# Performance work log

Hardware: AMD Instinct MI355X
Metric: run time of the kernel (lower is better)

The kernel has to match this reference:

```python
import jax, jax.numpy as jnp
import numpy as np

D_MODEL = 1024
NUM_HEADS = 16
HEAD_DIM = D_MODEL // NUM_HEADS


def setup_inputs() -> dict:
    key = jax.random.key(0)
    k1, k2, k3, k4, k5 = jax.random.split(key, 5)
    scale = 1.0 / np.sqrt(D_MODEL)
    x = jax.random.normal(k1, (2, 2048, D_MODEL), dtype=jnp.float32)
    Wqkv = jax.random.uniform(k2, (D_MODEL, 3 * D_MODEL), jnp.float32, -scale, scale)
    bqkv = jax.random.uniform(k3, (3 * D_MODEL,), jnp.float32, -scale, scale)
    Wout = jax.random.uniform(k4, (D_MODEL, D_MODEL), jnp.float32, -scale, scale)
    bout = jax.random.uniform(k5, (D_MODEL,), jnp.float32, -scale, scale)
    return {"x": x, "Wqkv": Wqkv, "bqkv": bqkv, "Wout": Wout, "bout": bout}


def reference(x, Wqkv, bqkv, Wout, bout):
    B, S, _ = x.shape
    qkv = x @ Wqkv + bqkv                                   # [B, S, 3*D]
    # reshape to [B, S, H, 3*head_dim] then to [B, H, S, 3*head_dim]
    qkv = qkv.reshape(B, S, NUM_HEADS, 3 * HEAD_DIM).transpose(0, 2, 1, 3)
    q, k, v = jnp.split(qkv, 3, axis=-1)                    # each [B, H, S, hd]
    scaled = jnp.einsum("bhqd,bhkd->bhqk", q, k) / jnp.sqrt(jnp.float32(HEAD_DIM))
    attn = jax.nn.softmax(scaled, axis=-1)                  # [B, H, S, S]
    values = jnp.einsum("bhqk,bhkd->bhqd", attn, v)         # [B, H, S, hd]
    values = values.transpose(0, 2, 1, 3).reshape(B, S, D_MODEL)
    return values @ Wout + bout
```

## Files before the change

kernel.cpp:

```cpp
#include <hip/hip_runtime.h>


typedef __attribute__((ext_vector_type(8)))  short short8;
typedef __attribute__((ext_vector_type(4)))  short short4v;
typedef __attribute__((ext_vector_type(8)))  float float8;
typedef __attribute__((ext_vector_type(4)))  float f32x4;
typedef __attribute__((ext_vector_type(16))) float f32x16;
typedef __attribute__((ext_vector_type(4)))  int   int4v;

#define D_MODEL 1024
#define NHEAD   16
#define HD      64
#define SEQ     2048
#define N3      (3*D_MODEL)
#define MB      (1024*1024)

static __device__ __forceinline__ float bf2f(short s) {
    unsigned u = ((unsigned)(unsigned short)s) << 16;
    return __builtin_bit_cast(float, u);
}
static __device__ __forceinline__ short f2bf(float f) {
    unsigned u = __builtin_bit_cast(unsigned, f);
    u = (u + 0x7fff + ((u >> 16) & 1)) >> 16;
    return (short)u;
}
static __device__ __forceinline__ unsigned pkbf(float a, float b) {
    unsigned ua = __builtin_bit_cast(unsigned, a);
    ua = (ua + 0x7fff + ((ua >> 16) & 1)) >> 16;
    unsigned ub = __builtin_bit_cast(unsigned, b);
    ub = (ub + 0x7fff + ((ub >> 16) & 1)) & 0xffff0000u;
    return ua | ub;
}
static __device__ __forceinline__ unsigned cvtpk(float a, float b) {
    unsigned r;
    asm("v_cvt_pk_bf16_f32 %0, %1, %2" : "=v"(r) : "v"(a), "v"(b));
    return r;
}
static __device__ __forceinline__ void gl16(const short* g, short* l) {
    __builtin_amdgcn_global_load_lds(
        (const __attribute__((address_space(1))) unsigned int*)g,
        (__attribute__((address_space(3))) unsigned int*)l, 16, 0, 0);
}

__global__ __launch_bounds__(256) void prep(
    const float* __restrict__ x, const float* __restrict__ Wqkv,
    const float* __restrict__ Wout,
    short* __restrict__ Xh, short* __restrict__ Xl,
    short* __restrict__ Wh, short* __restrict__ Wl,
    short* __restrict__ Woh, short* __restrict__ Wol)
{
    __shared__ float tile[32][33];
    const int bid = blockIdx.x;
    const int tid = threadIdx.x;

    if (bid < 2048) {
        const int i = (bid * 256 + tid) * 8;
        const float8 v = *(const float8*)&x[i];
        short8 h, l;
#pragma unroll
        for (int j = 0; j < 8; ++j) {
            h[j] = f2bf(v[j]);
            l[j] = f2bf(v[j] - bf2f(h[j]));
        }
        *(short8*)&Xh[i] = h;
        *(short8*)&Xl[i] = l;
        return;
    }

    const float* in; short *hi, *lo; int K, N, bx, by;
    if (bid < 5120) {
        const int b2 = bid - 2048;
        in = Wqkv; hi = Wh; lo = Wl; K = D_MODEL; N = N3;
        bx = b2 % 96; by = b2 / 96;
    } else {
        const int b3 = bid - 5120;
        in = Wout; hi = Woh; lo = Wol; K = D_MODEL; N = D_MODEL;
        bx = b3 & 31; by = b3 >> 5;
    }
    const int n0 = bx * 32, k0 = by * 32;
    const int tx = tid & 31, ty = tid >> 5;
#pragma unroll
    for (int i = 0; i < 4; ++i)
        tile[ty + 8*i][tx] = in[(k0 + ty + 8*i) * N + (n0 + tx)];
    __syncthreads();
#pragma unroll
    for (int i = 0; i < 4; ++i) {
        const float v  = tile[tx][ty + 8*i];
        const short vh = f2bf(v);
        const short vl = f2bf(v - bf2f(vh));
        const int idx  = (n0 + ty + 8*i) * K + (k0 + tx);
        hi[idx] = vh;
        lo[idx] = vl;
    }
}

#define QBUF_SH 28672
#define OFF_AL  8192
#define OFF_BH  16384
#define OFF_BL  22528

__global__ __launch_bounds__(512, 2) void qkv_gemm8(
    const short* __restrict__ Xh, const short* __restrict__ Xl,
    const short* __restrict__ Bh, const short* __restrict__ Bl,
    const float* __restrict__ bias,
    short* __restrict__ Qo, short* __restrict__ Ko, short* __restrict__ Vt)
{
    __shared__ __attribute__((aligned(16))) short smem[2 * QBUF_SH];

    const int tid  = threadIdx.x;
    const int wave = tid >> 6, lane = tid & 63;
    const int q4 = lane >> 4, l16 = lane & 15;
    const int wr = wave >> 2, wc = wave & 3;

    const int flat = blockIdx.x;
    const int sw = (flat & 7) * 32 + (flat >> 3);
    const int mt = sw & 15, nt = sw >> 4;
    const int m0 = mt * 256, n0 = nt * 192;

    const short* srcp[7];
#pragma unroll
    for (int j = 0; j < 7; ++j) {
        const int id = j * 512 + tid;
        const short* s;
        if (id < 1024)      { s = &Xh[(size_t)(m0 + (id >> 2)) * D_MODEL + (id & 3) * 8]; }
        else if (id < 2048) { const int c = id - 1024; s = &Xl[(size_t)(m0 + (c >> 2)) * D_MODEL + (c & 3) * 8]; }
        else if (id < 2816) { const int c = id - 2048; s = &Bh[(size_t)(n0 + (c >> 2)) * D_MODEL + (c & 3) * 8]; }
        else                { const int c = id - 2816; s = &Bl[(size_t)(n0 + (c >> 2)) * D_MODEL + (c & 3) * 8]; }
        srcp[j] = s;
    }

    auto stage = [&](int b) {
#pragma unroll
        for (int j = 0; j < 7; ++j) {
            gl16(srcp[j], smem + b * QBUF_SH + (j * 512 + tid) * 8);
            srcp[j] += 32;
        }
    };

    f32x4 acc[8][3];
#pragma unroll
    for (int i = 0; i < 8; ++i)
#pragma unroll
        for (int j = 0; j < 3; ++j) acc[i][j] = (f32x4){0.f, 0.f, 0.f, 0.f};

    stage(0);
    asm volatile("s_waitcnt vmcnt(0)" ::: "memory");
    __builtin_amdgcn_s_barrier();

    for (int t = 0; t < 32; ++t) {
        const int cur = t & 1;
        const short* base = smem + cur * QBUF_SH;
        const short* Ah_s = base;
        const short* Al_s = base + OFF_AL;
        const short* Bh_s = base + OFF_BH;
        const short* Bl_s = base + OFF_BL;

        short8 bhf[3], blf[3];
#pragma unroll
        for (int p = 0; p < 4; ++p) {
            const int r0 = (wr * 128 + (2*p)   * 16 + l16) * 32 + q4 * 8;
            const int r1 = (wr * 128 + (2*p+1) * 16 + l16) * 32 + q4 * 8;
            const short8 a0h = *(const short8*)(Ah_s + r0);
            const short8 a0l = *(const short8*)(Al_s + r0);
            const short8 a1h = *(const short8*)(Ah_s + r1);
            const short8 a1l = *(const short8*)(Al_s + r1);
            if (p == 0) {
#pragma unroll
                for (int n = 0; n < 3; ++n) {
                    const int rb = (wc * 48 + n * 16 + l16) * 32 + q4 * 8;
                    bhf[n] = *(const short8*)(Bh_s + rb);
                    blf[n] = *(const short8*)(Bl_s + rb);
                }
                if (t < 31) stage(cur ^ 1);
            }
            __builtin_amdgcn_s_barrier();
            asm volatile("s_waitcnt lgkmcnt(0)" ::: "memory");
            __builtin_amdgcn_sched_barrier(0);
            __builtin_amdgcn_s_setprio(1);
#pragma unroll
            for (int n = 0; n < 3; ++n) {
                acc[2*p][n]   = __builtin_amdgcn_mfma_f32_16x16x32_bf16(a0h, bhf[n], acc[2*p][n],   0, 0, 0);
                acc[2*p][n]   = __builtin_amdgcn_mfma_f32_16x16x32_bf16(a0h, blf[n], acc[2*p][n],   0, 0, 0);
                acc[2*p][n]   = __builtin_amdgcn_mfma_f32_16x16x32_bf16(a0l, bhf[n], acc[2*p][n],   0, 0, 0);
                acc[2*p+1][n] = __builtin_amdgcn_mfma_f32_16x16x32_bf16(a1h, bhf[n], acc[2*p+1][n], 0, 0, 0);
                acc[2*p+1][n] = __builtin_amdgcn_mfma_f32_16x16x32_bf16(a1h, blf[n], acc[2*p+1][n], 0, 0, 0);
                acc[2*p+1][n] = __builtin_amdgcn_mfma_f32_16x16x32_bf16(a1l, bhf[n], acc[2*p+1][n], 0, 0, 0);
            }
            __builtin_amdgcn_s_setprio(0);
            if (p == 3) asm volatile("s_waitcnt vmcnt(0)" ::: "memory");
            __builtin_amdgcn_s_barrier();
        }
    }

    const float SCALE_Q = 0.125f * 1.4426950408889634f;
#pragma unroll
    for (int tj = 0; tj < 3; ++tj) {
        const int jj = wc * 48 + tj * 16 + l16;
        const int n  = nt * 192 + jj;
        const float bv = bias[n];
#pragma unroll
        for (int ti = 0; ti < 8; ++ti) {
            const int mb = m0 + wr * 128 + ti * 16 + q4 * 4;
            const int b = mb >> 11;
            const int s = mb & 2047;
            const int bh_ = b * NHEAD + nt;
            if (jj >= 128) {
                short4v v4;
#pragma unroll
                for (int r = 0; r < 4; ++r) v4[r] = f2bf(acc[ti][tj][r] + bv);
                *(short4v*)&Vt[(bh_ * HD + (jj - 128)) * SEQ + s] = v4;
            } else if (jj < 64) {
#pragma unroll
                for (int r = 0; r < 4; ++r)
                    Qo[(bh_ * SEQ + s + r) * HD + jj] = f2bf((acc[ti][tj][r] + bv) * SCALE_Q);
            } else {
#pragma unroll
                for (int r = 0; r < 4; ++r)
                    Ko[(bh_ * SEQ + s + r) * HD + (jj - 64)] = f2bf(acc[ti][tj][r] + bv);
            }
        }
    }
}

__global__ __launch_bounds__(256, 2) void attn_tscore(
    const short* __restrict__ Q, const short* __restrict__ K,
    const short* __restrict__ Vt,
    short* __restrict__ Ch, short* __restrict__ Cl)
{
    __shared__ __attribute__((aligned(16))) char smem[36864];
    short (*Ks)[72] = (short(*)[72])smem;
    short (*Vs)[72] = (short(*)[72])(smem + 18432);

    const int bh = blockIdx.x;
    const int qb = blockIdx.y;
    const int bi = bh >> 4, hi_ = bh & 15;

    const short* Qp  = Q  + bh * SEQ * HD;
    const short* Kp  = K  + bh * SEQ * HD;
    const short* Vtp = Vt + bh * HD * SEQ;

    const int tid  = threadIdx.x;
    const int wave = tid >> 6, lane = tid & 63;
    const int l5 = lane & 31, hf = lane >> 5;
    const int q0w = qb * 128 + wave * 32;

    short8 qf[4];
#pragma unroll
    for (int c = 0; c < 4; ++c)
        qf[c] = *(const short8*)&Qp[(q0w + l5) * HD + c * 16 + hf * 8];

    f32x16 oacc0 = (f32x16)(0.f), oacc1 = (f32x16)(0.f);
    float m = -1.0e30f, l = 0.f;

    const int sr = tid >> 2;
    const int sc = (tid & 3) * 16;

    short8 kr0 = *(const short8*)&Kp[sr * HD + sc];
    short8 kr1 = *(const short8*)&Kp[sr * HD + sc + 8];
    short8 vr0 = *(const short8*)&Vtp[sr * SEQ + sc];
    short8 vr1 = *(const short8*)&Vtp[sr * SEQ + sc + 8];
    *(short8*)&Ks[sr][sc]     = kr0;
    *(short8*)&Ks[sr][sc + 8] = kr1;
    *(short8*)&Vs[sr][sc]     = vr0;
    *(short8*)&Vs[sr][sc + 8] = vr1;
    __syncthreads();

    for (int kc = 0; kc < 32; ++kc) {
        const int buf = (kc & 1) << 6;

        if (kc < 31) {
            const int nkb = (kc + 1) << 6;
            kr0 = *(const short8*)&Kp[(nkb + sr) * HD + sc];
            kr1 = *(const short8*)&Kp[(nkb + sr) * HD + sc + 8];
            vr0 = *(const short8*)&Vtp[sr * SEQ + nkb + sc];
            vr1 = *(const short8*)&Vtp[sr * SEQ + nkb + sc + 8];
        }

        f32x16 s0 = (f32x16)(0.f), s1 = (f32x16)(0.f);
#pragma unroll
        for (int c = 0; c < 4; ++c) {
            const short8 ka0 = *(const short8*)&Ks[buf + l5][c * 16 + hf * 8];
            const short8 ka1 = *(const short8*)&Ks[buf + 32 + l5][c * 16 + hf * 8];
            s0 = __builtin_amdgcn_mfma_f32_32x32x16_bf16(ka0, qf[c], s0, 0, 0, 0);
            s1 = __builtin_amdgcn_mfma_f32_32x32x16_bf16(ka1, qf[c], s1, 0, 0, 0);
        }

        float t[8];
#pragma unroll
        for (int i = 0; i < 8; ++i)
            t[i] = fmaxf(fmaxf(s0[i], s0[i + 8]), fmaxf(s1[i], s1[i + 8]));
        float pmax = fmaxf(fmaxf(fmaxf(t[0], t[1]), fmaxf(t[2], t[3])),
                           fmaxf(fmaxf(t[4], t[5]), fmaxf(t[6], t[7])));
        pmax = fmaxf(pmax, __shfl_xor(pmax, 32, 64));

        if (!__all(pmax - m <= 8.0f)) {
            const float mnew  = fmaxf(m, pmax);
            const float alpha = exp2f(m - mnew);
#pragma unroll
            for (int i = 0; i < 16; ++i) { oacc0[i] *= alpha; oacc1[i] *= alpha; }
            l *= alpha;
            m = mnew;
        }

        float p0[16], p1[16];
#pragma unroll
        for (int i = 0; i < 16; ++i) { p0[i] = exp2f(s0[i] - m); p1[i] = exp2f(s1[i] - m); }
        float sa = 0.f, sb = 0.f, sc_ = 0.f, sd = 0.f;
#pragma unroll
        for (int i = 0; i < 4; ++i) {
            sa += p0[i] + p0[i + 8];
            sb += p0[i + 4] + p0[i + 12];
            sc_ += p1[i] + p1[i + 8];
            sd += p1[i + 4] + p1[i + 12];
        }
        float rs = (sa + sb) + (sc_ + sd);
        rs += __shfl_xor(rs, 32, 64);
        l += rs;

        unsigned u0 = cvtpk(p0[0],  p0[1]),  u1 = cvtpk(p0[2],  p0[3]);
        unsigned u2 = cvtpk(p0[4],  p0[5]),  u3 = cvtpk(p0[6],  p0[7]);
        unsigned u4 = cvtpk(p0[8],  p0[9]),  u5 = cvtpk(p0[10], p0[11]);
        unsigned u6 = cvtpk(p0[12], p0[13]), u7 = cvtpk(p0[14], p0[15]);
        unsigned w0 = cvtpk(p1[0],  p1[1]),  w1 = cvtpk(p1[2],  p1[3]);
        unsigned w2 = cvtpk(p1[4],  p1[5]),  w3 = cvtpk(p1[6],  p1[7]);
        unsigned w4 = cvtpk(p1[8],  p1[9]),  w5 = cvtpk(p1[10], p1[11]);
        unsigned w6 = cvtpk(p1[12], p1[13]), w7 = cvtpk(p1[14], p1[15]);
        const unsigned x0 = __shfl_xor(u0, 32, 64), x1 = __shfl_xor(u1, 32, 64);
        const unsigned x2 = __shfl_xor(u2, 32, 64), x3 = __shfl_xor(u3, 32, 64);
        const unsigned x4 = __shfl_xor(u4, 32, 64), x5 = __shfl_xor(u5, 32, 64);
        const unsigned x6 = __shfl_xor(u6, 32, 64), x7 = __shfl_xor(u7, 32, 64);
        const unsigned y0 = __shfl_xor(w0, 32, 64), y1 = __shfl_xor(w1, 32, 64);
        const unsigned y2 = __shfl_xor(w2, 32, 64), y3 = __shfl_xor(w3, 32, 64);
        const unsigned y4 = __shfl_xor(w4, 32, 64), y5 = __shfl_xor(w5, 32, 64);
        const unsigned y6 = __shfl_xor(w6, 32, 64), y7 = __shfl_xor(w7, 32, 64);
        int4v pb0 = (int4v){ (int)(hf ? x2 : u0), (int)(hf ? x3 : u1),
                             (int)(hf ? u2 : x0), (int)(hf ? u3 : x1) };
        int4v pb1 = (int4v){ (int)(hf ? x6 : u4), (int)(hf ? x7 : u5),
                             (int)(hf ? u6 : x4), (int)(hf ? u7 : x5) };
        int4v pb2 = (int4v){ (int)(hf ? y2 : w0), (int)(hf ? y3 : w1),
                             (int)(hf ? w2 : y0), (int)(hf ? w3 : y1) };
        int4v pb3 = (int4v){ (int)(hf ? y6 : w4), (int)(hf ? y7 : w5),
                             (int)(hf ? w6 : y4), (int)(hf ? w7 : y5) };
        const short8 pbf0 = __builtin_bit_cast(short8, pb0);
        const short8 pbf1 = __builtin_bit_cast(short8, pb1);
        const short8 pbf2 = __builtin_bit_cast(short8, pb2);
        const short8 pbf3 = __builtin_bit_cast(short8, pb3);

        {
            const short8 va0 = *(const short8*)&Vs[buf + l5][hf * 8];
            const short8 va1 = *(const short8*)&Vs[buf + l5][16 + hf * 8];
            const short8 va2 = *(const short8*)&Vs[buf + l5][32 + hf * 8];
            const short8 va3 = *(const short8*)&Vs[buf + l5][48 + hf * 8];
            oacc0 = __builtin_amdgcn_mfma_f32_32x32x16_bf16(va0, pbf0, oacc0, 0, 0, 0);
            oacc0 = __builtin_amdgcn_mfma_f32_32x32x16_bf16(va1, pbf1, oacc0, 0, 0, 0);
            oacc0 = __builtin_amdgcn_mfma_f32_32x32x16_bf16(va2, pbf2, oacc0, 0, 0, 0);
            oacc0 = __builtin_amdgcn_mfma_f32_32x32x16_bf16(va3, pbf3, oacc0, 0, 0, 0);
            const short8 vb0 = *(const short8*)&Vs[buf + 32 + l5][hf * 8];
            const short8 vb1 = *(const short8*)&Vs[buf + 32 + l5][16 + hf * 8];
            const short8 vb2 = *(const short8*)&Vs[buf + 32 + l5][32 + hf * 8];
            const short8 vb3 = *(const short8*)&Vs[buf + 32 + l5][48 + hf * 8];
            oacc1 = __builtin_amdgcn_mfma_f32_32x32x16_bf16(vb0, pbf0, oacc1, 0, 0, 0);
            oacc1 = __builtin_amdgcn_mfma_f32_32x32x16_bf16(vb1, pbf1, oacc1, 0, 0, 0);
            oacc1 = __builtin_amdgcn_mfma_f32_32x32x16_bf16(vb2, pbf2, oacc1, 0, 0, 0);
            oacc1 = __builtin_amdgcn_mfma_f32_32x32x16_bf16(vb3, pbf3, oacc1, 0, 0, 0);
        }

        if (kc < 31) {
            const int wb = ((kc + 1) & 1) << 6;
            *(short8*)&Ks[wb + sr][sc]     = kr0;
            *(short8*)&Ks[wb + sr][sc + 8] = kr1;
            *(short8*)&Vs[wb + sr][sc]     = vr0;
            *(short8*)&Vs[wb + sr][sc + 8] = vr1;
        }
        __syncthreads();
    }

    const float inv = 1.0f / l;
#pragma unroll
    for (int i = 0; i < 16; ++i) { oacc0[i] *= inv; oacc1[i] *= inv; }

    float (*epi)[68] = (float(*)[68])(smem + wave * 8704);
#pragma unroll
    for (int r = 0; r < 16; ++r) {
        const int d = (r & 3) + 8 * (r >> 2) + 4 * hf;
        epi[l5][d]      = oacc0[r];
        epi[l5][32 + d] = oacc1[r];
    }
    __builtin_amdgcn_s_waitcnt(0);
#pragma unroll
    for (int pass = 0; pass < 8; ++pass) {
        const int row = pass * 4 + (lane >> 4);
        const int col = (lane & 15) * 4;
        const float4 v = *(const float4*)&epi[row][col];
        const float o[4] = {v.x, v.y, v.z, v.w};
        short4v hh, ll;
#pragma unroll
        for (int i = 0; i < 4; ++i) {
            hh[i] = f2bf(o[i]);
            ll[i] = f2bf(o[i] - bf2f(hh[i]));
        }
        const size_t co = ((size_t)(bi * SEQ + q0w + row)) * D_MODEL + hi_ * HD + col;
        *(short4v*)&Ch[co] = hh;
        *(short4v*)&Cl[co] = ll;
    }
}

__global__ __launch_bounds__(256) void out_gemm128(
    const short* __restrict__ Ah, const short* __restrict__ Al,
    const short* __restrict__ Bh, const short* __restrict__ Bl,
    const float* __restrict__ bias, float* __restrict__ out)
{
    __shared__ short AhS[128*32], AlS[128*32], BhS[128*32], BlS[128*32];

    const int tid  = threadIdx.x;
    const int wave = tid >> 6, lane = tid & 63;
    const int q4 = lane >> 4, l16 = lane & 15;
    const int m0 = blockIdx.y * 128, n0 = blockIdx.x * 128;
    const int rw = (wave & 1) * 64, cw = (wave >> 1) * 64;
    const int trow = tid >> 2;
    const int tcol = (tid & 3) * 8;

    f32x4 acc[4][4];
#pragma unroll
    for (int i = 0; i < 4; ++i)
#pragma unroll
        for (int j = 0; j < 4; ++j) acc[i][j] = (f32x4){0.f, 0.f, 0.f, 0.f};

    for (int kt = 0; kt < D_MODEL; kt += 32) {
        gl16(&Ah[(m0 + trow) * D_MODEL + kt + tcol],      AhS + tid * 8);
        gl16(&Ah[(m0 + 64 + trow) * D_MODEL + kt + tcol], AhS + 2048 + tid * 8);
        gl16(&Al[(m0 + trow) * D_MODEL + kt + tcol],      AlS + tid * 8);
        gl16(&Al[(m0 + 64 + trow) * D_MODEL + kt + tcol], AlS + 2048 + tid * 8);
        gl16(&Bh[(n0 + trow) * D_MODEL + kt + tcol],      BhS + tid * 8);
        gl16(&Bh[(n0 + 64 + trow) * D_MODEL + kt + tcol], BhS + 2048 + tid * 8);
        gl16(&Bl[(n0 + trow) * D_MODEL + kt + tcol],      BlS + tid * 8);
        gl16(&Bl[(n0 + 64 + trow) * D_MODEL + kt + tcol], BlS + 2048 + tid * 8);
        __syncthreads();

        short8 ah[4], al[4], bh[4], bl[4];
#pragma unroll
        for (int t = 0; t < 4; ++t) {
            ah[t] = *(const short8*)&AhS[(rw + t * 16 + l16) * 32 + q4 * 8];
            al[t] = *(const short8*)&AlS[(rw + t * 16 + l16) * 32 + q4 * 8];
            bh[t] = *(const short8*)&BhS[(cw + t * 16 + l16) * 32 + q4 * 8];
            bl[t] = *(const short8*)&BlS[(cw + t * 16 + l16) * 32 + q4 * 8];
        }
#pragma unroll
        for (int ti = 0; ti < 4; ++ti)
#pragma unroll
            for (int tj = 0; tj < 4; ++tj) {
                acc[ti][tj] = __builtin_amdgcn_mfma_f32_16x16x32_bf16(ah[ti], bh[tj], acc[ti][tj], 0, 0, 0);
                acc[ti][tj] = __builtin_amdgcn_mfma_f32_16x16x32_bf16(ah[ti], bl[tj], acc[ti][tj], 0, 0, 0);
                acc[ti][tj] = __builtin_amdgcn_mfma_f32_16x16x32_bf16(al[ti], bh[tj], acc[ti][tj], 0, 0, 0);
            }
        __syncthreads();
    }

#pragma unroll
    for (int tj = 0; tj < 4; ++tj) {
        const int n = n0 + cw + tj * 16 + l16;
        const float bv = bias[n];
#pragma unroll
        for (int ti = 0; ti < 4; ++ti) {
            const int mb = m0 + rw + ti * 16 + q4 * 4;
#pragma unroll
            for (int r = 0; r < 4; ++r)
                out[(mb + r) * D_MODEL + n] = acc[ti][tj][r] + bv;
        }
    }
}

extern "C" void kernel_launch(void* const* d_in, const int* in_sizes, int n_in,
                              void* d_out, int out_size, void* d_ws, size_t ws_size,
                              hipStream_t stream)
{
    const float* x    = (const float*)d_in[0];
    const float* Wqkv = (const float*)d_in[1];
    const float* bqkv = (const float*)d_in[2];
    const float* Wout = (const float*)d_in[3];
    const float* bout = (const float*)d_in[4];
    float* out = (float*)d_out;

    char* ws = (char*)d_ws;
    short* Qb  = (short*)(ws);
    short* Kb  = (short*)(ws +  8*MB);
    short* Vtb = (short*)(ws + 16*MB);
    short* Woh = (short*)(ws + 24*MB);
    short* Wol = (short*)(ws + 26*MB);
    short* Ch  = (short*)(ws + 28*MB);
    short* Cl  = (short*)(ws + 36*MB);
    short* Xh  = (short*)(ws + 44*MB);
    short* Xl  = (short*)(ws + 52*MB);
    short* Wh  = (short*)(ws + 60*MB);
    short* Wl  = (short*)(ws + 66*MB);

    prep<<<6144, 256, 0, stream>>>(x, Wqkv, Wout, Xh, Xl, Wh, Wl, Woh, Wol);
    qkv_gemm8<<<dim3(256), 512, 0, stream>>>(Xh, Xl, Wh, Wl, bqkv, Qb, Kb, Vtb);
    attn_tscore<<<dim3(32, 16), 256, 0, stream>>>(Qb, Kb, Vtb, Ch, Cl);
    out_gemm128<<<dim3(8, 32), 256, 0, stream>>>(Ch, Cl, Woh, Wol, bout, out);
}
```

Before: 280.1 us.

## Swizzle LDS tile layout in QKV and output GEMMs and restructure QKV k-loop phases

Applies an XOR swizzle to the column group of each 16-byte chunk when staging A/B tiles into LDS and when reading MFMA fragments, in both the QKV GEMM and the output-projection GEMM, to reduce LDS bank conflicts on the short8 fragment reads. The QKV GEMM inner loop is also reorganised from four sub-phases into two halves. Each half loads four A fragment pairs at once and issues its MFMAs, so there are fewer barriers per k-step. This raises register pressure from the extra held fragments under the 512-thread, 2-block launch bounds. An unused bf16 packing helper is removed.

```diff
diff --git a/kernel.cpp b/kernel.cpp
--- a/kernel.cpp
+++ b/kernel.cpp
@@ -23,13 +23,6 @@
     unsigned u = __builtin_bit_cast(unsigned, f);
     u = (u + 0x7fff + ((u >> 16) & 1)) >> 16;
     return (short)u;
-}
-static __device__ __forceinline__ unsigned pkbf(float a, float b) {
-    unsigned ua = __builtin_bit_cast(unsigned, a);
-    ua = (ua + 0x7fff + ((ua >> 16) & 1)) >> 16;
-    unsigned ub = __builtin_bit_cast(unsigned, b);
-    ub = (ub + 0x7fff + ((ub >> 16) & 1)) & 0xffff0000u;
-    return ua | ub;
 }
 static __device__ __forceinline__ unsigned cvtpk(float a, float b) {
     unsigned r;
@@ -111,6 +104,7 @@
     const int wave = tid >> 6, lane = tid & 63;
     const int q4 = lane >> 4, l16 = lane & 15;
     const int wr = wave >> 2, wc = wave & 3;
+    const int csw = (q4 ^ ((l16 ^ (l16 >> 2)) & 3)) * 8;
 
     const int flat = blockIdx.x;
     const int sw = (flat & 7) * 32 + (flat >> 3);
@@ -121,12 +115,13 @@
 #pragma unroll
     for (int j = 0; j < 7; ++j) {
         const int id = j * 512 + tid;
-        const short* s;
-        if (id < 1024)      { s = &Xh[(size_t)(m0 + (id >> 2)) * D_MODEL + (id & 3) * 8]; }
-        else if (id < 2048) { const int c = id - 1024; s = &Xl[(size_t)(m0 + (c >> 2)) * D_MODEL + (c & 3) * 8]; }
-        else if (id < 2816) { const int c = id - 2048; s = &Bh[(size_t)(n0 + (c >> 2)) * D_MODEL + (c & 3) * 8]; }
-        else                { const int c = id - 2816; s = &Bl[(size_t)(n0 + (c >> 2)) * D_MODEL + (c & 3) * 8]; }
-        srcp[j] = s;
+        int r; const short* mat; int row0;
+        if (id < 1024)      { r = id >> 2;          mat = Xh; row0 = m0; }
+        else if (id < 2048) { r = (id - 1024) >> 2; mat = Xl; row0 = m0; }
+        else if (id < 2816) { r = (id - 2048) >> 2; mat = Bh; row0 = n0; }
+        else                { r = (id - 2816) >> 2; mat = Bl; row0 = n0; }
+        const int cg = (id & 3) ^ ((r ^ (r >> 2)) & 3);
+        srcp[j] = &mat[(size_t)(row0 + r) * D_MODEL + cg * 8];
     }
 
     auto stage = [&](int b) {
@@ -155,41 +150,57 @@
         const short* Bh_s = base + OFF_BH;
         const short* Bl_s = base + OFF_BL;
 
-        short8 bhf[3], blf[3];
-#pragma unroll
-        for (int p = 0; p < 4; ++p) {
-            const int r0 = (wr * 128 + (2*p)   * 16 + l16) * 32 + q4 * 8;
-            const int r1 = (wr * 128 + (2*p+1) * 16 + l16) * 32 + q4 * 8;
-            const short8 a0h = *(const short8*)(Ah_s + r0);
-            const short8 a0l = *(const short8*)(Al_s + r0);
-            const short8 a1h = *(const short8*)(Ah_s + r1);
-            const short8 a1l = *(const short8*)(Al_s + r1);
-            if (p == 0) {
-#pragma unroll
-                for (int n = 0; n < 3; ++n) {
-                    const int rb = (wc * 48 + n * 16 + l16) * 32 + q4 * 8;
-                    bhf[n] = *(const short8*)(Bh_s + rb);
-                    blf[n] = *(const short8*)(Bl_s + rb);
-                }
-                if (t < 31) stage(cur ^ 1);
+        short8 bhf[3], blf[3], a0h[4], a0l[4];
+#pragma unroll
+        for (int n = 0; n < 3; ++n) {
+            const int rb = (wc * 48 + n * 16 + l16) * 32 + csw;
+            bhf[n] = *(const short8*)(Bh_s + rb);
+            blf[n] = *(const short8*)(Bl_s + rb);
+        }
+#pragma unroll
+        for (int ti = 0; ti < 4; ++ti) {
+            const int ra = (wr * 128 + ti * 16 + l16) * 32 + csw;
+            a0h[ti] = *(const short8*)(Ah_s + ra);
+            a0l[ti] = *(const short8*)(Al_s + ra);
+        }
+        if (t < 31) stage(cur ^ 1);
+        __builtin_amdgcn_s_barrier();
+        asm volatile("s_waitcnt lgkmcnt(0)" ::: "memory");
+        __builtin_amdgcn_sched_barrier(0);
+        short8 a1h[4], a1l[4];
+#pragma unroll
+        for (int ti = 0; ti < 4; ++ti) {
+            const int ra = (wr * 128 + (4 + ti) * 16 + l16) * 32 + csw;
+            a1h[ti] = *(const short8*)(Ah_s + ra);
+            a1l[ti] = *(const short8*)(Al_s + ra);
+        }
+        __builtin_amdgcn_sched_barrier(0);
+        __builtin_amdgcn_s_setprio(1);
+#pragma unroll
+        for (int ti = 0; ti < 4; ++ti)
+#pragma unroll
+            for (int n = 0; n < 3; ++n) {
+                acc[ti][n] = __builtin_amdgcn_mfma_f32_16x16x32_bf16(a0h[ti], bhf[n], acc[ti][n], 0, 0, 0);
+                acc[ti][n] = __builtin_amdgcn_mfma_f32_16x16x32_bf16(a0h[ti], blf[n], acc[ti][n], 0, 0, 0);
+                acc[ti][n] = __builtin_amdgcn_mfma_f32_16x16x32_bf16(a0l[ti], bhf[n], acc[ti][n], 0, 0, 0);
             }
-            __builtin_amdgcn_s_barrier();
-            asm volatile("s_waitcnt lgkmcnt(0)" ::: "memory");
-            __builtin_amdgcn_sched_barrier(0);
-            __builtin_amdgcn_s_setprio(1);
+        __builtin_amdgcn_s_setprio(0);
+        __builtin_amdgcn_s_barrier();
+
+        asm volatile("s_waitcnt lgkmcnt(0)" ::: "memory");
+        __builtin_amdgcn_sched_barrier(0);
+        __builtin_amdgcn_s_setprio(1);
+#pragma unroll
+        for (int ti = 0; ti < 4; ++ti)
 #pragma unroll
             for (int n = 0; n < 3; ++n) {
-                acc[2*p][n]   = __builtin_amdgcn_mfma_f32_16x16x32_bf16(a0h, bhf[n], acc[2*p][n],   0, 0, 0);
-                acc[2*p][n]   = __builtin_amdgcn_mfma_f32_16x16x32_bf16(a0h, blf[n], acc[2*p][n],   0, 0, 0);
-                acc[2*p][n]   = __builtin_amdgcn_mfma_f32_16x16x32_bf16(a0l, bhf[n], acc[2*p][n],   0, 0, 0);
-                acc[2*p+1][n] = __builtin_amdgcn_mfma_f32_16x16x32_bf16(a1h, bhf[n], acc[2*p+1][n], 0, 0, 0);
-                acc[2*p+1][n] = __builtin_amdgcn_mfma_f32_16x16x32_bf16(a1h, blf[n], acc[2*p+1][n], 0, 0, 0);
-                acc[2*p+1][n] = __builtin_amdgcn_mfma_f32_16x16x32_bf16(a1l, bhf[n], acc[2*p+1][n], 0, 0, 0);
+                acc[4+ti][n] = __builtin_amdgcn_mfma_f32_16x16x32_bf16(a1h[ti], bhf[n], acc[4+ti][n], 0, 0, 0);
+                acc[4+ti][n] = __builtin_amdgcn_mfma_f32_16x16x32_bf16(a1h[ti], blf[n], acc[4+ti][n], 0, 0, 0);
+                acc[4+ti][n] = __builtin_amdgcn_mfma_f32_16x16x32_bf16(a1l[ti], bhf[n], acc[4+ti][n], 0, 0, 0);
             }
-            __builtin_amdgcn_s_setprio(0);
-            if (p == 3) asm volatile("s_waitcnt vmcnt(0)" ::: "memory");
-            __builtin_amdgcn_s_barrier();
-        }
+        __builtin_amdgcn_s_setprio(0);
+        asm volatile("s_waitcnt vmcnt(0)" ::: "memory");
+        __builtin_amdgcn_s_barrier();
     }
 
     const float SCALE_Q = 0.125f * 1.4426950408889634f;
@@ -418,7 +429,8 @@
     const int m0 = blockIdx.y * 128, n0 = blockIdx.x * 128;
     const int rw = (wave & 1) * 64, cw = (wave >> 1) * 64;
     const int trow = tid >> 2;
-    const int tcol = (tid & 3) * 8;
+    const int tcol = (((tid & 3) ^ ((trow ^ (trow >> 2)) & 3))) * 8;
+    const int csw = (q4 ^ ((l16 ^ (l16 >> 2)) & 3)) * 8;
 
     f32x4 acc[4][4];
 #pragma unroll
@@ -440,10 +452,12 @@
         short8 ah[4], al[4], bh[4], bl[4];
 #pragma unroll
         for (int t = 0; t < 4; ++t) {
-            ah[t] = *(const short8*)&AhS[(rw + t * 16 + l16) * 32 + q4 * 8];
-            al[t] = *(const short8*)&AlS[(rw + t * 16 + l16) * 32 + q4 * 8];
-            bh[t] = *(const short8*)&BhS[(cw + t * 16 + l16) * 32 + q4 * 8];
-            bl[t] = *(const short8*)&BlS[(cw + t * 16 + l16) * 32 + q4 * 8];
+            const int ra = (rw + t * 16 + l16) * 32 + csw;
+            const int rb = (cw + t * 16 + l16) * 32 + csw;
+            ah[t] = *(const short8*)&AhS[ra];
+            al[t] = *(const short8*)&AlS[ra];
+            bh[t] = *(const short8*)&BhS[rb];
+            bl[t] = *(const short8*)&BlS[rb];
         }
 #pragma unroll
         for (int ti = 0; ti < 4; ++ti)
```

Measured after the change: 276.1 us. Within noise of the previous version (-1.4%).
